# Kernel tuning notes

Measured on AMD Instinct MI355X. Metric: run time of the kernel, lower is better.

Reference implementation:

```python
import jax, jax.numpy as jnp
import numpy as np

NC = 80            # number of classes (COCO)
NM = 32            # mask coefficients (YOLOv5-seg)
D = 4 + 1 + NC + NM
N_ANCHORS = 100800  # 1280x1280 input, strides 8/16/32, 3 anchors
CONF_THRES = 0.25
IOU_THRES = 0.45
MAX_DET = 300
TOPK = 4096        # fixed pre-NMS candidate budget (jit-compatible stand-in for boolean filter)


def setup_inputs() -> dict:
    key = jax.random.key(0)
    x = jax.random.uniform(key, (1, N_ANCHORS, D), dtype=jnp.float32)
    return {"x": x}


def _pairwise_iou(boxes):
    # boxes: [K, 4] in (y1, x1, y2, x2)
    y1, x1, y2, x2 = boxes[:, 0], boxes[:, 1], boxes[:, 2], boxes[:, 3]
    area = (y2 - y1) * (x2 - x1)
    iy1 = jnp.maximum(y1[:, None], y1[None, :])
    ix1 = jnp.maximum(x1[:, None], x1[None, :])
    iy2 = jnp.minimum(y2[:, None], y2[None, :])
    ix2 = jnp.minimum(x2[:, None], x2[None, :])
    inter = jnp.clip(iy2 - iy1, 0.0) * jnp.clip(ix2 - ix1, 0.0)
    union = area[:, None] + area[None, :] - inter
    return inter / jnp.maximum(union, 1e-9)


def reference(x):
    p = x[0]                                   # [N, D] (loop returns after first image)
    obj = p[:, 4]
    valid = obj > CONF_THRES                   # candidates = obj score > conf_thres
    cls_scores = p[:, 5:5 + NC] * obj[:, None] # scores = cls * obj
    scores = jnp.max(cls_scores, axis=1)
    classes = jnp.argmax(cls_scores, axis=1).astype(x.dtype)
    # xywh (center) -> yxyx
    xc, yc, w, h = p[:, 0], p[:, 1], p[:, 2], p[:, 3]
    yxyx = jnp.stack([yc - h * 0.5, xc - w * 0.5, yc + h * 0.5, xc + w * 0.5], axis=1)
    masks = p[:, 5 + NC:]                      # [N, NM]
    # replace torch's boolean-filter gather with fixed-size top-K over masked scores
    scores_m = jnp.where(valid, scores, -1.0)
    top_s, top_i = jax.lax.top_k(scores_m, TOPK)   # sorted desc, as torchvision nms requires
    b = yxyx[top_i]                            # [K, 4]
    keep0 = top_s > -0.5                       # only real candidates
    iou = _pairwise_iou(b)                     # [K, K]
    j_idx = jnp.arange(TOPK)

    def body(i, keep):
        sup = keep[i] & (iou[i] > IOU_THRES) & (j_idx > i)
        return keep & ~sup

    keep = jax.lax.fori_loop(0, TOPK, body, keep0)
    # pad/select top MAX_DET surviving detections (score -1.0 marks padding)
    sel_s = jnp.where(keep, top_s, -1.0)
    out_s, out_i = jax.lax.top_k(sel_s, MAX_DET)
    gi = top_i[out_i]
    return (yxyx[gi][None], classes[gi][None], out_s[None], masks[gi][None])
```

## Files before the change

### kernel.cpp

```cpp
#include <hip/hip_runtime.h>


#define AS1 __attribute__((address_space(1)))
#define AS3 __attribute__((address_space(3)))

constexpr int    N_ANCH = 100800;
constexpr int    DIMV   = 117;
constexpr int    NCLS   = 80;
constexpr int    TOPKN  = 4096;
constexpr int    MAXDET = 300;
constexpr int    KCAP   = 12288;
constexpr int    NBUCK  = 16384;
constexpr int    NSLICE = 32;

constexpr size_t WS_HIST   = 0;
constexpr size_t WS_SCORES = WS_HIST   + 65536ull * 4;
constexpr size_t WS_CLS    = WS_SCORES + 100800ull * 4;
constexpr size_t WS_SEL    = WS_CLS    + 100800ull * 4;
constexpr size_t WS_KEYS   = WS_SEL    + 256;
constexpr size_t WS_RANK   = WS_KEYS   + (size_t)KCAP * 8;
constexpr size_t WS_SIDX   = WS_RANK   + (size_t)KCAP * 4;
constexpr size_t WS_SSC    = WS_SIDX   + 4096ull * 4;
constexpr size_t WS_BOXES  = WS_SSC    + 4096ull * 4;
constexpr size_t WS_MASK   = WS_BOXES  + 4096ull * 16;
constexpr size_t WS_OUTI   = WS_MASK   + 4096ull * 64 * 8;
constexpr size_t WS_OUTS   = WS_OUTI   + 1200;

__global__ void zero_kernel(unsigned* __restrict__ slices, int* __restrict__ sel,
                            int* __restrict__ rank) {
    int i = blockIdx.x * blockDim.x + threadIdx.x;
    if (i < NSLICE * NBUCK) slices[i] = 0u;
    if (i < KCAP)           rank[i]  = 0;
    if (i < 64)             sel[i]   = 0;
}

constexpr int SROWS = 64;
__global__ void score_kernel(const float* __restrict__ x, float* __restrict__ scores,
                             int* __restrict__ cls, unsigned* __restrict__ slices) {
    __shared__ float sx[SROWS * DIMV];
    int block0 = blockIdx.x * SROWS;
    const float4* src = (const float4*)(x + (size_t)block0 * DIMV);
    float4* dst = (float4*)sx;
    constexpr int NV4 = SROWS * DIMV / 4;
    for (int i = threadIdx.x; i < NV4; i += 128) dst[i] = src[i];
    __syncthreads();
    int row  = threadIdx.x >> 1;
    int half = threadIdx.x & 1;
    const float* rp = sx + row * DIMV;
    float obj = rp[4];
    const float* cp = rp + 5 + half * 40;
    float best = -1.0f;
    int   bc   = half * 40;
#pragma unroll 8
    for (int c = 0; c < 40; ++c) {
        float s = __fmul_rn(cp[c], obj);
        if (s > best) { best = s; bc = half * 40 + c; }
    }
    float so = __shfl_xor(best, 1);
    int   co = __shfl_xor(bc, 1);
    if (half == 0) {
        if (so > best) { best = so; bc = co; }
        int a = block0 + row;
        bool valid = obj > 0.25f;
        scores[a] = valid ? best : -1.0f;
        cls[a]    = bc;
        if (valid) {
            unsigned b = __float_as_uint(best) >> 16;
            atomicAdd(&slices[(blockIdx.x & (NSLICE - 1)) * NBUCK + b], 1u);
        }
    }
}

__global__ void reduce_hist_kernel(const unsigned* __restrict__ slices,
                                   unsigned* __restrict__ hist) {
    int b = blockIdx.x * 256 + threadIdx.x;
    unsigned s = 0;
#pragma unroll
    for (int k = 0; k < NSLICE; ++k) s += slices[k * NBUCK + b];
    hist[b] = s;
}

__global__ void select_kernel(const unsigned* __restrict__ hist, int* sel) {
    __shared__ unsigned sv[1024];
    int t = threadIdx.x;
    int base = NBUCK - 16 * (t + 1);
    const uint4* hp = (const uint4*)(hist + base);
    unsigned own = 0;
#pragma unroll
    for (int k = 0; k < 4; ++k) {
        uint4 v = hp[k];
        own += v.x + v.y + v.z + v.w;
    }
    sv[t] = own;
    __syncthreads();
    for (int off = 1; off < 1024; off <<= 1) {
        unsigned v = (t >= off) ? sv[t - off] : 0u;
        __syncthreads();
        sv[t] += v;
        __syncthreads();
    }
    unsigned incl = sv[t];
    unsigned before = incl - own;
    if (before < (unsigned)TOPKN && incl >= (unsigned)TOPKN) {
        unsigned running = before;
        for (int k = 15; k >= 0; --k) {
            unsigned h = hist[base + k];
            running += h;
            if (running >= (unsigned)TOPKN) {
                sel[0] = base + k;
                sel[1] = (int)(running - h);
                break;
            }
        }
    }
}

__global__ void compact_kernel(const float* __restrict__ scores, int* sel,
                               unsigned long long* __restrict__ keys) {
    int a = blockIdx.x * blockDim.x + threadIdx.x;
    if (a >= N_ANCH) return;
    float s = scores[a];
    if (s < 0.0f) return;
    unsigned bits = __float_as_uint(s);
    if ((int)(bits >> 16) < sel[0]) return;
    int pos = atomicAdd(&sel[2], 1);
    if (pos < KCAP) keys[pos] = ((unsigned long long)bits << 32) | (unsigned)(~a);
}

constexpr int NCOLP = 4;
__global__ void rank_kernel(const unsigned long long* __restrict__ keys,
                            const int* __restrict__ sel, int* __restrict__ rank) {
    __shared__ unsigned long long tile[2048];
    int n = sel[2]; if (n > KCAP) n = KCAP;
    int i = blockIdx.x * 256 + threadIdx.x;
    unsigned long long myKey = (i < n) ? keys[i] : 0ull;
    int cnt = 0;
    for (int t0 = blockIdx.y * 2048; t0 < n; t0 += 2048 * NCOLP) {
        int m = n - t0; if (m > 2048) m = 2048;
        for (int j = threadIdx.x; j < m; j += 256) tile[j] = keys[t0 + j];
        __syncthreads();
        int j = 0;
        for (; j + 3 < m; j += 4) {
            cnt += (tile[j]     > myKey);
            cnt += (tile[j + 1] > myKey);
            cnt += (tile[j + 2] > myKey);
            cnt += (tile[j + 3] > myKey);
        }
        for (; j < m; ++j) cnt += (tile[j] > myKey);
        __syncthreads();
    }
    if (i < n && cnt < TOPKN) atomicAdd(&rank[i], cnt);
}

__global__ void scatter_kernel(const float* __restrict__ x,
                               const unsigned long long* __restrict__ keys,
                               const int* __restrict__ sel, const int* __restrict__ rank,
                               int* __restrict__ sidx, float* __restrict__ sscore,
                               float* __restrict__ boxes) {
    int n = sel[2]; if (n > KCAP) n = KCAP;
    int i = blockIdx.x * 256 + threadIdx.x;
    if (i >= n) return;
    int r = rank[i];
    if (r >= TOPKN) return;
    unsigned long long k = keys[i];
    int a = (int)(~(unsigned)(k & 0xFFFFFFFFull));
    sidx[r]   = a;
    sscore[r] = __uint_as_float((unsigned)(k >> 32));
    const float* p = x + (size_t)a * DIMV;
    float xc = p[0], yc = p[1], w = p[2], h = p[3];
    float hw = __fmul_rn(w, 0.5f);
    float hh = __fmul_rn(h, 0.5f);
    boxes[r * 4 + 0] = __fsub_rn(yc, hh);
    boxes[r * 4 + 1] = __fsub_rn(xc, hw);
    boxes[r * 4 + 2] = __fadd_rn(yc, hh);
    boxes[r * 4 + 3] = __fadd_rn(xc, hw);
}

__global__ void iou_mask_kernel(const float* __restrict__ boxes,
                                unsigned long long* __restrict__ mask) {
    int colT = blockIdx.x, rowT = blockIdx.y;
    int t = threadIdx.x;
    int r = rowT * 64 + t;
    if (colT < rowT) {
        mask[(size_t)r * 64 + colT] = 0ull;
        return;
    }
    __shared__ float cb[64][5];
    int cj = colT * 64 + t;
    {
        float y1 = boxes[cj * 4 + 0], x1 = boxes[cj * 4 + 1];
        float y2 = boxes[cj * 4 + 2], x2 = boxes[cj * 4 + 3];
        cb[t][0] = y1; cb[t][1] = x1; cb[t][2] = y2; cb[t][3] = x2;
        cb[t][4] = __fmul_rn(__fsub_rn(y2, y1), __fsub_rn(x2, x1));
    }
    __syncthreads();
    float ry1 = boxes[r * 4 + 0], rx1 = boxes[r * 4 + 1];
    float ry2 = boxes[r * 4 + 2], rx2 = boxes[r * 4 + 3];
    float rarea = __fmul_rn(__fsub_rn(ry2, ry1), __fsub_rn(rx2, rx1));
    unsigned long long bitsw = 0ull;
#pragma unroll 8
    for (int j = 0; j < 64; ++j) {
        float iy1 = fmaxf(ry1, cb[j][0]);
        float ix1 = fmaxf(rx1, cb[j][1]);
        float iy2 = fminf(ry2, cb[j][2]);
        float ix2 = fminf(rx2, cb[j][3]);
        float ih = fmaxf(__fsub_rn(iy2, iy1), 0.0f);
        float iw = fmaxf(__fsub_rn(ix2, ix1), 0.0f);
        float inter = __fmul_rn(ih, iw);
        float uni = __fsub_rn(__fadd_rn(rarea, cb[j][4]), inter);
        float iou = __fdiv_rn(inter, fmaxf(uni, 1e-9f));
        if (iou > 0.45f && (colT * 64 + j) > r) bitsw |= (1ull << j);
    }
    mask[(size_t)r * 64 + colT] = bitsw;
}

__global__ void __launch_bounds__(64, 1)
nms_scan_kernel(const unsigned long long* __restrict__ mask,
                const float* __restrict__ sscore,
                int* __restrict__ outIdx, float* __restrict__ outScore) {
    int lane = threadIdx.x;
    unsigned long long remv = 0ull;
    __shared__ __align__(16) unsigned long long tile[2 * 4096];
    __shared__ int keepArr[MAXDET];
    __shared__ unsigned long long remvFinal[64];
    int count = 0;

    auto issueBatch = [&](int w) {
        const char* gbase = (const char*)mask + (size_t)w * 32768 + (size_t)lane * 16;
        char* lbase = (char*)tile + (size_t)(w & 1) * 32768;
#pragma unroll
        for (int i = 0; i < 32; ++i) {
            __builtin_amdgcn_global_load_lds(
                (AS1 const unsigned*)(gbase + (size_t)i * 1024),
                (AS3 unsigned*)(lbase + (size_t)i * 1024), 16, 0, 0);
        }
    };

    issueBatch(0);
    for (int w = 0; w < 64 && count < MAXDET; ++w) {
        if (w + 1 < 64) issueBatch(w + 1);
        unsigned long long cand = __shfl(~remv, w);
        if (!cand) continue;
        asm volatile("s_waitcnt vmcnt(32)" ::: "memory");
        const unsigned long long* trow = tile + (size_t)(w & 1) * 4096;
        while (cand && count < MAXDET) {
            int bs[8];
            unsigned long long c2 = cand;
            int g = 0;
#pragma unroll
            for (int t = 0; t < 8; ++t) {
                bs[t] = c2 ? (int)__builtin_ctzll(c2) : 0;
                if (c2) { c2 &= c2 - 1; g = t + 1; }
            }
            unsigned long long mvs[8];
#pragma unroll
            for (int t = 0; t < 8; ++t) {
                mvs[t] = trow[(size_t)bs[t] * 64 + lane];
            }
#pragma unroll
            for (int t = 0; t < 8; ++t) {
                if (t < g && count < MAXDET) {
                    int b = bs[t];
                    unsigned long long bal = __ballot(((remv >> b) & 1ull) != 0);
                    if (!((bal >> w) & 1ull)) {
                        if (lane == 0) keepArr[count] = (w << 6) + b;
                        count++;
                        remv |= mvs[t];
                    }
                }
            }
            cand = c2;
        }
    }
    __syncthreads();
    remvFinal[lane] = remv;
    __syncthreads();
    int K = count;
    for (int k = lane; k < K; k += 64) {
        int s = keepArr[k];
        outIdx[k] = s;
        outScore[k] = sscore[s];
    }
    if (K < MAXDET && lane == 0) {
        int filled = K;
        for (int w = 0; w < 64 && filled < MAXDET; ++w) {
            unsigned long long word = remvFinal[w];
            while (word && filled < MAXDET) {
                int b = (int)__builtin_ctzll(word);
                word &= word - 1;
                outIdx[filled] = (w << 6) + b;
                outScore[filled] = -1.0f;
                filled++;
            }
        }
    }
}

__global__ void write_out_kernel(const float* __restrict__ x, const int* __restrict__ sidx,
                                 const int* __restrict__ cls, const float* __restrict__ boxes,
                                 const int* __restrict__ outIdx, const float* __restrict__ outScore,
                                 float* __restrict__ out) {
    int o = blockIdx.x;
    int t = threadIdx.x;
    int s = outIdx[o];
    int a = sidx[s];
    if (t < 32) {
        out[1800 + o * 32 + t] = x[(size_t)a * DIMV + 85 + t];
    } else if (t < 36) {
        out[o * 4 + (t - 32)] = boxes[s * 4 + (t - 32)];
    } else if (t == 36) {
        out[1200 + o] = (float)cls[a];
    } else if (t == 37) {
        out[1500 + o] = outScore[o];
    }
}

extern "C" void kernel_launch(void* const* d_in, const int* in_sizes, int n_in,
                              void* d_out, int out_size, void* d_ws, size_t ws_size,
                              hipStream_t stream) {
    const float* x = (const float*)d_in[0];
    char* ws = (char*)d_ws;
    unsigned*            hist   = (unsigned*)(ws + WS_HIST);
    float*               scores = (float*)(ws + WS_SCORES);
    int*                 cls    = (int*)(ws + WS_CLS);
    int*                 sel    = (int*)(ws + WS_SEL);
    unsigned long long*  keys   = (unsigned long long*)(ws + WS_KEYS);
    int*                 rank   = (int*)(ws + WS_RANK);
    int*                 sidx   = (int*)(ws + WS_SIDX);
    float*               sscore = (float*)(ws + WS_SSC);
    float*               boxes  = (float*)(ws + WS_BOXES);
    unsigned long long*  mask   = (unsigned long long*)(ws + WS_MASK);
    unsigned*            slices = (unsigned*)(ws + WS_MASK);
    int*                 outIdx = (int*)(ws + WS_OUTI);
    float*               outSc  = (float*)(ws + WS_OUTS);

    zero_kernel<<<(NSLICE * NBUCK + 255) / 256, 256, 0, stream>>>(slices, sel, rank);
    score_kernel<<<N_ANCH / SROWS, 128, 0, stream>>>(x, scores, cls, slices);
    reduce_hist_kernel<<<NBUCK / 256, 256, 0, stream>>>(slices, hist);
    select_kernel<<<1, 1024, 0, stream>>>(hist, sel);
    compact_kernel<<<(N_ANCH + 255) / 256, 256, 0, stream>>>(scores, sel, keys);
    dim3 rg(KCAP / 256, NCOLP);
    rank_kernel<<<rg, 256, 0, stream>>>(keys, sel, rank);
    scatter_kernel<<<KCAP / 256, 256, 0, stream>>>(x, keys, sel, rank, sidx, sscore, boxes);
    dim3 mg(64, 64);
    iou_mask_kernel<<<mg, 64, 0, stream>>>(boxes, mask);
    nms_scan_kernel<<<1, 64, 0, stream>>>(mask, sscore, outIdx, outSc);
    write_out_kernel<<<MAXDET, 64, 0, stream>>>(x, sidx, cls, boxes, outIdx, outSc, (float*)d_out);
}
```

Measured before the change: 216.6 us.

## Pack upper-triangular NMS mask, fold histogram reduce into select, restructure scan

Stores only the upper-triangular IoU mask tiles in a packed layout plus a separate diagonal copy. The NMS scan now resolves each 64-box word from the diagonal using readlanes and only ORs kept rows' packed tiles, so it streams about half as much data into LDS. It also fuses the histogram reduction into select (with fewer slices), moves rank zeroing into compact, and splits rank into one tile per block with early exits. The per-iteration waitcnt switch and packed indexing add complexity and carry a risk of off-by-one errors.

New measurement: 247.3 us. +14.2%, slower.

```diff
diff --git a/kernel.cpp b/kernel.cpp
--- a/kernel.cpp
+++ b/kernel.cpp
@@ -6,32 +6,32 @@
 
 constexpr int    N_ANCH = 100800;
 constexpr int    DIMV   = 117;
-constexpr int    NCLS   = 80;
 constexpr int    TOPKN  = 4096;
 constexpr int    MAXDET = 300;
 constexpr int    KCAP   = 12288;
 constexpr int    NBUCK  = 16384;
-constexpr int    NSLICE = 32;
-
-constexpr size_t WS_HIST   = 0;
-constexpr size_t WS_SCORES = WS_HIST   + 65536ull * 4;
-constexpr size_t WS_CLS    = WS_SCORES + 100800ull * 4;
-constexpr size_t WS_SEL    = WS_CLS    + 100800ull * 4;
+constexpr int    NSLICE = 8;
+
+constexpr int PACK_TOT = 133120;
+
+constexpr size_t WS_SLICES = 0;
+constexpr size_t WS_SCORES = WS_SLICES + (size_t)NSLICE * NBUCK * 4;
+constexpr size_t WS_CLS    = WS_SCORES + (size_t)N_ANCH * 4;
+constexpr size_t WS_SEL    = WS_CLS    + (size_t)N_ANCH * 4;
 constexpr size_t WS_KEYS   = WS_SEL    + 256;
 constexpr size_t WS_RANK   = WS_KEYS   + (size_t)KCAP * 8;
 constexpr size_t WS_SIDX   = WS_RANK   + (size_t)KCAP * 4;
 constexpr size_t WS_SSC    = WS_SIDX   + 4096ull * 4;
 constexpr size_t WS_BOXES  = WS_SSC    + 4096ull * 4;
-constexpr size_t WS_MASK   = WS_BOXES  + 4096ull * 16;
-constexpr size_t WS_OUTI   = WS_MASK   + 4096ull * 64 * 8;
-constexpr size_t WS_OUTS   = WS_OUTI   + 1200;
-
-__global__ void zero_kernel(unsigned* __restrict__ slices, int* __restrict__ sel,
-                            int* __restrict__ rank) {
-    int i = blockIdx.x * blockDim.x + threadIdx.x;
+constexpr size_t WS_MASKP  = WS_BOXES  + 4096ull * 16;
+constexpr size_t WS_DIAG   = WS_MASKP  + (size_t)PACK_TOT * 8 + 4096;
+constexpr size_t WS_OUTI   = WS_DIAG   + 4096ull * 8;
+constexpr size_t WS_OUTS   = WS_OUTI   + 1280;
+
+__global__ void zero_kernel(unsigned* __restrict__ slices, int* __restrict__ sel) {
+    int i = blockIdx.x * 256 + threadIdx.x;
     if (i < NSLICE * NBUCK) slices[i] = 0u;
-    if (i < KCAP)           rank[i]  = 0;
-    if (i < 64)             sel[i]   = 0;
+    if (i < 64)             sel[i]    = 0;
 }
 
 constexpr int SROWS = 64;
@@ -71,26 +71,25 @@
     }
 }
 
-__global__ void reduce_hist_kernel(const unsigned* __restrict__ slices,
-                                   unsigned* __restrict__ hist) {
-    int b = blockIdx.x * 256 + threadIdx.x;
-    unsigned s = 0;
-#pragma unroll
-    for (int k = 0; k < NSLICE; ++k) s += slices[k * NBUCK + b];
-    hist[b] = s;
-}
-
-__global__ void select_kernel(const unsigned* __restrict__ hist, int* sel) {
+__global__ void select_kernel(const unsigned* __restrict__ slices, int* sel) {
     __shared__ unsigned sv[1024];
     int t = threadIdx.x;
     int base = NBUCK - 16 * (t + 1);
-    const uint4* hp = (const uint4*)(hist + base);
+    unsigned hb[16];
+#pragma unroll
+    for (int k = 0; k < 16; ++k) hb[k] = 0u;
+    for (int s = 0; s < NSLICE; ++s) {
+        const uint4* hp = (const uint4*)(slices + (size_t)s * NBUCK + base);
+#pragma unroll
+        for (int q = 0; q < 4; ++q) {
+            uint4 v = hp[q];
+            hb[q * 4 + 0] += v.x; hb[q * 4 + 1] += v.y;
+            hb[q * 4 + 2] += v.z; hb[q * 4 + 3] += v.w;
+        }
+    }
     unsigned own = 0;
 #pragma unroll
-    for (int k = 0; k < 4; ++k) {
-        uint4 v = hp[k];
-        own += v.x + v.y + v.z + v.w;
-    }
+    for (int k = 0; k < 16; ++k) own += hb[k];
     sv[t] = own;
     __syncthreads();
     for (int off = 1; off < 1024; off <<= 1) {
@@ -104,11 +103,10 @@
     if (before < (unsigned)TOPKN && incl >= (unsigned)TOPKN) {
         unsigned running = before;
         for (int k = 15; k >= 0; --k) {
-            unsigned h = hist[base + k];
-            running += h;
+            running += hb[k];
             if (running >= (unsigned)TOPKN) {
                 sel[0] = base + k;
-                sel[1] = (int)(running - h);
+                sel[1] = (int)(running - hb[k]);
                 break;
             }
         }
@@ -116,8 +114,10 @@
 }
 
 __global__ void compact_kernel(const float* __restrict__ scores, int* sel,
-                               unsigned long long* __restrict__ keys) {
+                               unsigned long long* __restrict__ keys,
+                               int* __restrict__ rank) {
     int a = blockIdx.x * blockDim.x + threadIdx.x;
+    if (a < KCAP) rank[a] = 0;
     if (a >= N_ANCH) return;
     float s = scores[a];
     if (s < 0.0f) return;
@@ -127,29 +127,29 @@
     if (pos < KCAP) keys[pos] = ((unsigned long long)bits << 32) | (unsigned)(~a);
 }
 
-constexpr int NCOLP = 4;
+constexpr int NCOLP = 8;
 __global__ void rank_kernel(const unsigned long long* __restrict__ keys,
                             const int* __restrict__ sel, int* __restrict__ rank) {
     __shared__ unsigned long long tile[2048];
     int n = sel[2]; if (n > KCAP) n = KCAP;
+    if (blockIdx.x * 256 >= n) return;
+    int t0 = blockIdx.y * 2048;
+    if (t0 >= n) return;
     int i = blockIdx.x * 256 + threadIdx.x;
     unsigned long long myKey = (i < n) ? keys[i] : 0ull;
+    int m = n - t0; if (m > 2048) m = 2048;
+    for (int j = threadIdx.x; j < m; j += 256) tile[j] = keys[t0 + j];
+    __syncthreads();
     int cnt = 0;
-    for (int t0 = blockIdx.y * 2048; t0 < n; t0 += 2048 * NCOLP) {
-        int m = n - t0; if (m > 2048) m = 2048;
-        for (int j = threadIdx.x; j < m; j += 256) tile[j] = keys[t0 + j];
-        __syncthreads();
-        int j = 0;
-        for (; j + 3 < m; j += 4) {
-            cnt += (tile[j]     > myKey);
-            cnt += (tile[j + 1] > myKey);
-            cnt += (tile[j + 2] > myKey);
-            cnt += (tile[j + 3] > myKey);
-        }
-        for (; j < m; ++j) cnt += (tile[j] > myKey);
-        __syncthreads();
-    }
-    if (i < n && cnt < TOPKN) atomicAdd(&rank[i], cnt);
+    int j = 0;
+    for (; j + 3 < m; j += 4) {
+        cnt += (tile[j]     > myKey);
+        cnt += (tile[j + 1] > myKey);
+        cnt += (tile[j + 2] > myKey);
+        cnt += (tile[j + 3] > myKey);
+    }
+    for (; j < m; ++j) cnt += (tile[j] > myKey);
+    if (i < n && cnt) atomicAdd(&rank[i], cnt);
 }
 
 __global__ void scatter_kernel(const float* __restrict__ x,
@@ -177,25 +177,23 @@
 }
 
 __global__ void iou_mask_kernel(const float* __restrict__ boxes,
-                                unsigned long long* __restrict__ mask) {
+                                unsigned long long* __restrict__ maskp,
+                                unsigned long long* __restrict__ diag) {
     int colT = blockIdx.x, rowT = blockIdx.y;
+    if (colT < rowT) return;
     int t = threadIdx.x;
-    int r = rowT * 64 + t;
-    if (colT < rowT) {
-        mask[(size_t)r * 64 + colT] = 0ull;
-        return;
-    }
     __shared__ float cb[64][5];
+    const float4* bp = (const float4*)boxes;
     int cj = colT * 64 + t;
     {
-        float y1 = boxes[cj * 4 + 0], x1 = boxes[cj * 4 + 1];
-        float y2 = boxes[cj * 4 + 2], x2 = boxes[cj * 4 + 3];
-        cb[t][0] = y1; cb[t][1] = x1; cb[t][2] = y2; cb[t][3] = x2;
-        cb[t][4] = __fmul_rn(__fsub_rn(y2, y1), __fsub_rn(x2, x1));
-    }
-    __syncthreads();
-    float ry1 = boxes[r * 4 + 0], rx1 = boxes[r * 4 + 1];
-    float ry2 = boxes[r * 4 + 2], rx2 = boxes[r * 4 + 3];
+        float4 c = bp[cj];
+        cb[t][0] = c.x; cb[t][1] = c.y; cb[t][2] = c.z; cb[t][3] = c.w;
+        cb[t][4] = __fmul_rn(__fsub_rn(c.z, c.x), __fsub_rn(c.w, c.y));
+    }
+    __syncthreads();
+    int r = rowT * 64 + t;
+    float4 rv = bp[r];
+    float ry1 = rv.x, rx1 = rv.y, ry2 = rv.z, rx2 = rv.w;
     float rarea = __fmul_rn(__fsub_rn(ry2, ry1), __fsub_rn(rx2, rx1));
     unsigned long long bitsw = 0ull;
 #pragma unroll 8
@@ -211,65 +209,105 @@
         float iou = __fdiv_rn(inter, fmaxf(uni, 1e-9f));
         if (iou > 0.45f && (colT * 64 + j) > r) bitsw |= (1ull << j);
     }
-    mask[(size_t)r * 64 + colT] = bitsw;
+    int pb = 64 * (64 * rowT - (rowT * (rowT - 1)) / 2);
+    maskp[pb + t * (64 - rowT) + (colT - rowT)] = bitsw;
+    if (colT == rowT) diag[(rowT << 6) + t] = bitsw;
+}
+
+__device__ __forceinline__ unsigned long long readlane64(unsigned long long v, int l) {
+    unsigned lo = (unsigned)__builtin_amdgcn_readlane((int)(unsigned)(v & 0xFFFFFFFFull), l);
+    unsigned hi = (unsigned)__builtin_amdgcn_readlane((int)(unsigned)(v >> 32), l);
+    return ((unsigned long long)hi << 32) | lo;
 }
 
 __global__ void __launch_bounds__(64, 1)
-nms_scan_kernel(const unsigned long long* __restrict__ mask,
+nms_scan_kernel(const unsigned long long* __restrict__ maskp,
+                const unsigned long long* __restrict__ diagG,
                 const float* __restrict__ sscore,
                 int* __restrict__ outIdx, float* __restrict__ outScore) {
     int lane = threadIdx.x;
     unsigned long long remv = 0ull;
     __shared__ __align__(16) unsigned long long tile[2 * 4096];
+    __shared__ __align__(16) unsigned long long diagLds[4096];
     __shared__ int keepArr[MAXDET];
     __shared__ unsigned long long remvFinal[64];
     int count = 0;
 
     auto issueBatch = [&](int w) {
-        const char* gbase = (const char*)mask + (size_t)w * 32768 + (size_t)lane * 16;
+        if (w >= 64) return;
+        int L = (65 - w) >> 1;
+        const char* gbase = (const char*)maskp +
+                            (size_t)(64 * (64 * w - (w * (w - 1)) / 2)) * 8 +
+                            (size_t)lane * 16;
         char* lbase = (char*)tile + (size_t)(w & 1) * 32768;
-#pragma unroll
-        for (int i = 0; i < 32; ++i) {
+        for (int i = 0; i < L; ++i) {
             __builtin_amdgcn_global_load_lds(
                 (AS1 const unsigned*)(gbase + (size_t)i * 1024),
                 (AS3 unsigned*)(lbase + (size_t)i * 1024), 16, 0, 0);
         }
     };
 
+    {
+        const char* gb = (const char*)diagG + (size_t)lane * 16;
+        char* lb = (char*)diagLds;
+#pragma unroll
+        for (int i = 0; i < 32; ++i) {
+            __builtin_amdgcn_global_load_lds(
+                (AS1 const unsigned*)(gb + (size_t)i * 1024),
+                (AS3 unsigned*)(lb + (size_t)i * 1024), 16, 0, 0);
+        }
+    }
     issueBatch(0);
+
+#define VW(n) asm volatile("s_waitcnt vmcnt(" #n ")" ::: "memory")
+
     for (int w = 0; w < 64 && count < MAXDET; ++w) {
-        if (w + 1 < 64) issueBatch(w + 1);
+        issueBatch(w + 1);
         unsigned long long cand = __shfl(~remv, w);
         if (!cand) continue;
-        asm volatile("s_waitcnt vmcnt(32)" ::: "memory");
+        int p = (w < 63) ? ((64 - w) >> 1) : 0;
+        switch (p) {
+            case 32: VW(32); break; case 31: VW(31); break; case 30: VW(30); break;
+            case 29: VW(29); break; case 28: VW(28); break; case 27: VW(27); break;
+            case 26: VW(26); break; case 25: VW(25); break; case 24: VW(24); break;
+            case 23: VW(23); break; case 22: VW(22); break; case 21: VW(21); break;
+            case 20: VW(20); break; case 19: VW(19); break; case 18: VW(18); break;
+            case 17: VW(17); break; case 16: VW(16); break; case 15: VW(15); break;
+            case 14: VW(14); break; case 13: VW(13); break; case 12: VW(12); break;
+            case 11: VW(11); break; case 10: VW(10); break; case  9: VW(9);  break;
+            case  8: VW(8);  break; case  7: VW(7);  break; case  6: VW(6);  break;
+            case  5: VW(5);  break; case  4: VW(4);  break; case  3: VW(3);  break;
+            case  2: VW(2);  break; case  1: VW(1);  break; default: VW(0);  break;
+        }
+        unsigned long long diagv = diagLds[(w << 6) | lane];
+        unsigned long long alive = cand;
+        unsigned long long keptM = 0ull;
+        while (alive && count < MAXDET) {
+            int b = (int)__builtin_ctzll(alive);
+            unsigned long long db = readlane64(diagv, b);
+            if (lane == 0) keepArr[count] = (w << 6) + b;
+            count++;
+            keptM |= (1ull << b);
+            alive &= ~(db | (1ull << b));
+        }
         const unsigned long long* trow = tile + (size_t)(w & 1) * 4096;
-        while (cand && count < MAXDET) {
-            int bs[8];
-            unsigned long long c2 = cand;
-            int g = 0;
-#pragma unroll
-            for (int t = 0; t < 8; ++t) {
-                bs[t] = c2 ? (int)__builtin_ctzll(c2) : 0;
-                if (c2) { c2 &= c2 - 1; g = t + 1; }
+        int stride = 64 - w;
+        int rel = lane - w;
+        while (keptM) {
+            int bs[4]; unsigned long long t2 = keptM; int g = 0;
+#pragma unroll
+            for (int t = 0; t < 4; ++t) {
+                bs[t] = t2 ? (int)__builtin_ctzll(t2) : 0;
+                if (t2) { t2 &= t2 - 1; g = t + 1; }
             }
-            unsigned long long mvs[8];
-#pragma unroll
-            for (int t = 0; t < 8; ++t) {
-                mvs[t] = trow[(size_t)bs[t] * 64 + lane];
-            }
-#pragma unroll
-            for (int t = 0; t < 8; ++t) {
-                if (t < g && count < MAXDET) {
-                    int b = bs[t];
-                    unsigned long long bal = __ballot(((remv >> b) & 1ull) != 0);
-                    if (!((bal >> w) & 1ull)) {
-                        if (lane == 0) keepArr[count] = (w << 6) + b;
-                        count++;
-                        remv |= mvs[t];
-                    }
-                }
-            }
-            cand = c2;
+            unsigned long long vs[4];
+#pragma unroll
+            for (int t = 0; t < 4; ++t)
+                vs[t] = (rel >= 0) ? trow[bs[t] * stride + rel] : 0ull;
+#pragma unroll
+            for (int t = 0; t < 4; ++t)
+                if (t < g) remv |= vs[t];
+            keptM = t2;
         }
     }
     __syncthreads();
@@ -320,7 +358,7 @@
                               hipStream_t stream) {
     const float* x = (const float*)d_in[0];
     char* ws = (char*)d_ws;
-    unsigned*            hist   = (unsigned*)(ws + WS_HIST);
+    unsigned*            slices = (unsigned*)(ws + WS_SLICES);
     float*               scores = (float*)(ws + WS_SCORES);
     int*                 cls    = (int*)(ws + WS_CLS);
     int*                 sel    = (int*)(ws + WS_SEL);
@@ -329,21 +367,20 @@
     int*                 sidx   = (int*)(ws + WS_SIDX);
     float*               sscore = (float*)(ws + WS_SSC);
     float*               boxes  = (float*)(ws + WS_BOXES);
-    unsigned long long*  mask   = (unsigned long long*)(ws + WS_MASK);
-    unsigned*            slices = (unsigned*)(ws + WS_MASK);
+    unsigned long long*  maskp  = (unsigned long long*)(ws + WS_MASKP);
+    unsigned long long*  diag   = (unsigned long long*)(ws + WS_DIAG);
     int*                 outIdx = (int*)(ws + WS_OUTI);
     float*               outSc  = (float*)(ws + WS_OUTS);
 
-    zero_kernel<<<(NSLICE * NBUCK + 255) / 256, 256, 0, stream>>>(slices, sel, rank);
+    zero_kernel<<<(NSLICE * NBUCK) / 256, 256, 0, stream>>>(slices, sel);
     score_kernel<<<N_ANCH / SROWS, 128, 0, stream>>>(x, scores, cls, slices);
-    reduce_hist_kernel<<<NBUCK / 256, 256, 0, stream>>>(slices, hist);
-    select_kernel<<<1, 1024, 0, stream>>>(hist, sel);
-    compact_kernel<<<(N_ANCH + 255) / 256, 256, 0, stream>>>(scores, sel, keys);
+    select_kernel<<<1, 1024, 0, stream>>>(slices, sel);
+    compact_kernel<<<(N_ANCH + 255) / 256, 256, 0, stream>>>(scores, sel, keys, rank);
     dim3 rg(KCAP / 256, NCOLP);
     rank_kernel<<<rg, 256, 0, stream>>>(keys, sel, rank);
     scatter_kernel<<<KCAP / 256, 256, 0, stream>>>(x, keys, sel, rank, sidx, sscore, boxes);
     dim3 mg(64, 64);
-    iou_mask_kernel<<<mg, 64, 0, stream>>>(boxes, mask);
-    nms_scan_kernel<<<1, 64, 0, stream>>>(mask, sscore, outIdx, outSc);
+    iou_mask_kernel<<<mg, 64, 0, stream>>>(boxes, maskp, diag);
+    nms_scan_kernel<<<1, 64, 0, stream>>>(maskp, diag, sscore, outIdx, outSc);
     write_out_kernel<<<MAXDET, 64, 0, stream>>>(x, sidx, cls, boxes, outIdx, outSc, (float*)d_out);
 }
```

## Fuse NMS pipeline into one persistent kernel with software grid barriers

Applied to the files above, without the earlier changes.

Replaces the chain of ten kernel launches with a single persistent 256-block kernel that separates its phases with atomic grid barriers, plus a small init kernel. It also switches to per-block shared-memory histograms, packs the IoU mask as an upper triangle only, and rewrites the NMS scan as a greedy next-alive-candidate search with prefetched mask rows. The aim is to remove launch overhead and the zero-fill and reduce passes. In exchange, phases such as ranking now run on fewer parallel blocks, and the spin barriers depend on all 256 blocks being co-resident.

Measured after the change: 815.0 us. 3.76x slower.

```diff
diff --git a/kernel.cpp b/kernel.cpp
--- a/kernel.cpp
+++ b/kernel.cpp
@@ -1,317 +1,354 @@
 #include <hip/hip_runtime.h>
 
 
-#define AS1 __attribute__((address_space(1)))
-#define AS3 __attribute__((address_space(3)))
-
-constexpr int    N_ANCH = 100800;
-constexpr int    DIMV   = 117;
-constexpr int    NCLS   = 80;
-constexpr int    TOPKN  = 4096;
-constexpr int    MAXDET = 300;
-constexpr int    KCAP   = 12288;
-constexpr int    NBUCK  = 16384;
-constexpr int    NSLICE = 32;
+typedef unsigned long long u64;
+
+constexpr int N_ANCH = 100800;
+constexpr int DIMV   = 117;
+constexpr int NCLS   = 80;
+constexpr int TOPKN  = 4096;
+constexpr int MAXDET = 300;
+constexpr int KCAP   = 12288;
+constexpr int NBUCK  = 16384;
+constexpr int NBLK   = 256;
+constexpr int NTHR   = 256;
+constexpr int GSIZE  = NBLK * NTHR;
+
+constexpr int NTILE2 = 2080;
 
 constexpr size_t WS_HIST   = 0;
-constexpr size_t WS_SCORES = WS_HIST   + 65536ull * 4;
-constexpr size_t WS_CLS    = WS_SCORES + 100800ull * 4;
-constexpr size_t WS_SEL    = WS_CLS    + 100800ull * 4;
-constexpr size_t WS_KEYS   = WS_SEL    + 256;
+constexpr size_t WS_BAR    = WS_HIST   + 65536;
+constexpr size_t WS_SEL    = WS_BAR    + 128;
+constexpr size_t WS_SARR   = WS_SEL    + 256;
+constexpr size_t WS_SCORES = WS_SARR   + 1472;
+constexpr size_t WS_CLS    = WS_SCORES + (size_t)N_ANCH * 4;
+constexpr size_t WS_KEYS   = WS_CLS    + (size_t)N_ANCH * 4;
 constexpr size_t WS_RANK   = WS_KEYS   + (size_t)KCAP * 8;
 constexpr size_t WS_SIDX   = WS_RANK   + (size_t)KCAP * 4;
 constexpr size_t WS_SSC    = WS_SIDX   + 4096ull * 4;
 constexpr size_t WS_BOXES  = WS_SSC    + 4096ull * 4;
-constexpr size_t WS_MASK   = WS_BOXES  + 4096ull * 16;
-constexpr size_t WS_OUTI   = WS_MASK   + 4096ull * 64 * 8;
-constexpr size_t WS_OUTS   = WS_OUTI   + 1200;
-
-__global__ void zero_kernel(unsigned* __restrict__ slices, int* __restrict__ sel,
-                            int* __restrict__ rank) {
-    int i = blockIdx.x * blockDim.x + threadIdx.x;
-    if (i < NSLICE * NBUCK) slices[i] = 0u;
-    if (i < KCAP)           rank[i]  = 0;
-    if (i < 64)             sel[i]   = 0;
-}
-
-constexpr int SROWS = 64;
-__global__ void score_kernel(const float* __restrict__ x, float* __restrict__ scores,
-                             int* __restrict__ cls, unsigned* __restrict__ slices) {
-    __shared__ float sx[SROWS * DIMV];
-    int block0 = blockIdx.x * SROWS;
-    const float4* src = (const float4*)(x + (size_t)block0 * DIMV);
-    float4* dst = (float4*)sx;
-    constexpr int NV4 = SROWS * DIMV / 4;
-    for (int i = threadIdx.x; i < NV4; i += 128) dst[i] = src[i];
+constexpr size_t WS_MASKP  = WS_BOXES  + 4096ull * 16;
+
+__global__ void init_kernel(unsigned* __restrict__ hist, int* __restrict__ sel,
+                            unsigned* __restrict__ bar) {
+    int i = blockIdx.x * 256 + threadIdx.x;
+    if (i < NBUCK) hist[i] = 0u;
+    if (i < 64)    sel[i]  = 0;
+    if (i < 32)    bar[i]  = 0u;
+}
+
+__device__ __forceinline__ void gridbar(unsigned* bar, int phase) {
     __syncthreads();
-    int row  = threadIdx.x >> 1;
-    int half = threadIdx.x & 1;
-    const float* rp = sx + row * DIMV;
-    float obj = rp[4];
-    const float* cp = rp + 5 + half * 40;
-    float best = -1.0f;
-    int   bc   = half * 40;
+    if (threadIdx.x == 0) {
+        __threadfence();
+        __hip_atomic_fetch_add(&bar[phase], 1u, __ATOMIC_ACQ_REL,
+                               __HIP_MEMORY_SCOPE_AGENT);
+        while (__hip_atomic_load(&bar[phase], __ATOMIC_ACQUIRE,
+                                 __HIP_MEMORY_SCOPE_AGENT) < (unsigned)NBLK) {
+            __builtin_amdgcn_s_sleep(2);
+        }
+        __threadfence();
+    }
+    __syncthreads();
+}
+
+__device__ __forceinline__ u64 readlane64(u64 v, int l) {
+    unsigned lo = (unsigned)__builtin_amdgcn_readlane((int)(unsigned)(v & 0xFFFFFFFFull), l);
+    unsigned hi = (unsigned)__builtin_amdgcn_readlane((int)(unsigned)(v >> 32), l);
+    return ((u64)hi << 32) | lo;
+}
+
+__global__ void __launch_bounds__(NTHR, 1)
+mega_kernel(const float* __restrict__ x, float* __restrict__ out,
+            char* __restrict__ ws) {
+    unsigned* hist   = (unsigned*)(ws + WS_HIST);
+    unsigned* bar    = (unsigned*)(ws + WS_BAR);
+    int*      sel    = (int*)(ws + WS_SEL);
+    int*      sArrG  = (int*)(ws + WS_SARR);
+    float*    scores = (float*)(ws + WS_SCORES);
+    int*      cls    = (int*)(ws + WS_CLS);
+    u64*      keys   = (u64*)(ws + WS_KEYS);
+    int*      rank   = (int*)(ws + WS_RANK);
+    int*      sidx   = (int*)(ws + WS_SIDX);
+    float*    sscore = (float*)(ws + WS_SSC);
+    float*    boxes  = (float*)(ws + WS_BOXES);
+    u64*      maskp  = (u64*)(ws + WS_MASKP);
+
+    __shared__ __align__(16) char smem[125440];
+
+    {
+        float*    sx = (float*)smem;
+        unsigned* lh = (unsigned*)(smem + 59904);
+        for (int i = threadIdx.x; i < NBUCK; i += NTHR) lh[i] = 0u;
+        __syncthreads();
+        constexpr int TROWS = 128;
+        constexpr int NTILE = (N_ANCH + TROWS - 1) / TROWS;
+        for (int tile = blockIdx.x; tile < NTILE; tile += NBLK) {
+            int r0 = tile * TROWS;
+            int rows = N_ANCH - r0; if (rows > TROWS) rows = TROWS;
+            const float4* src = (const float4*)(x + (size_t)r0 * DIMV);
+            float4* dst = (float4*)sx;
+            int nv4 = rows * DIMV / 4;
+            for (int i = threadIdx.x; i < nv4; i += NTHR) dst[i] = src[i];
+            __syncthreads();
+            int row = threadIdx.x >> 1, half = threadIdx.x & 1;
+            if (row < rows) {
+                const float* rp = sx + row * DIMV;
+                float obj = rp[4];
+                const float* cp = rp + 5 + half * 40;
+                float best = -1.0f; int bc = half * 40;
 #pragma unroll 8
-    for (int c = 0; c < 40; ++c) {
-        float s = __fmul_rn(cp[c], obj);
-        if (s > best) { best = s; bc = half * 40 + c; }
-    }
-    float so = __shfl_xor(best, 1);
-    int   co = __shfl_xor(bc, 1);
-    if (half == 0) {
-        if (so > best) { best = so; bc = co; }
-        int a = block0 + row;
-        bool valid = obj > 0.25f;
-        scores[a] = valid ? best : -1.0f;
-        cls[a]    = bc;
-        if (valid) {
-            unsigned b = __float_as_uint(best) >> 16;
-            atomicAdd(&slices[(blockIdx.x & (NSLICE - 1)) * NBUCK + b], 1u);
-        }
-    }
-}
-
-__global__ void reduce_hist_kernel(const unsigned* __restrict__ slices,
-                                   unsigned* __restrict__ hist) {
-    int b = blockIdx.x * 256 + threadIdx.x;
-    unsigned s = 0;
+                for (int c = 0; c < 40; ++c) {
+                    float s = __fmul_rn(cp[c], obj);
+                    if (s > best) { best = s; bc = half * 40 + c; }
+                }
+                float so = __shfl_xor(best, 1);
+                int   co = __shfl_xor(bc, 1);
+                if (half == 0) {
+                    if (so > best) { best = so; bc = co; }
+                    int a = r0 + row;
+                    bool valid = obj > 0.25f;
+                    scores[a] = valid ? best : -1.0f;
+                    cls[a] = bc;
+                    if (valid) atomicAdd(&lh[__float_as_uint(best) >> 16], 1u);
+                }
+            }
+            __syncthreads();
+        }
+        for (int b = threadIdx.x; b < NBUCK; b += NTHR) {
+            unsigned v = lh[b];
+            if (v) atomicAdd(&hist[b], v);
+        }
+    }
+    gridbar(bar, 0);
+
+    if (blockIdx.x == 0) {
+        unsigned* sv = (unsigned*)smem;
+        int* bsh = (int*)(smem + 2048);
+        int t = threadIdx.x;
+        int base = NBUCK - 64 * (t + 1);
+        const uint4* hp = (const uint4*)(hist + base);
+        unsigned own = 0;
 #pragma unroll
-    for (int k = 0; k < NSLICE; ++k) s += slices[k * NBUCK + b];
-    hist[b] = s;
-}
-
-__global__ void select_kernel(const unsigned* __restrict__ hist, int* sel) {
-    __shared__ unsigned sv[1024];
-    int t = threadIdx.x;
-    int base = NBUCK - 16 * (t + 1);
-    const uint4* hp = (const uint4*)(hist + base);
-    unsigned own = 0;
+        for (int q = 0; q < 16; ++q) { uint4 v = hp[q]; own += v.x + v.y + v.z + v.w; }
+        sv[t] = own;
+        __syncthreads();
+        for (int off = 1; off < 256; off <<= 1) {
+            unsigned v = (t >= off) ? sv[t - off] : 0u;
+            __syncthreads();
+            sv[t] += v;
+            __syncthreads();
+        }
+        unsigned incl = sv[t], before = incl - own;
+        if (before < (unsigned)TOPKN && incl >= (unsigned)TOPKN) {
+            bsh[0] = t; bsh[1] = (int)before;
+        }
+        __syncthreads();
+        if (t == 0) {
+            int ts = bsh[0];
+            unsigned running = (unsigned)bsh[1];
+            int cbase = NBUCK - 64 * (ts + 1);
+            unsigned hh[64];
 #pragma unroll
-    for (int k = 0; k < 4; ++k) {
-        uint4 v = hp[k];
-        own += v.x + v.y + v.z + v.w;
-    }
-    sv[t] = own;
-    __syncthreads();
-    for (int off = 1; off < 1024; off <<= 1) {
-        unsigned v = (t >= off) ? sv[t - off] : 0u;
-        __syncthreads();
-        sv[t] += v;
-        __syncthreads();
-    }
-    unsigned incl = sv[t];
-    unsigned before = incl - own;
-    if (before < (unsigned)TOPKN && incl >= (unsigned)TOPKN) {
-        unsigned running = before;
-        for (int k = 15; k >= 0; --k) {
-            unsigned h = hist[base + k];
-            running += h;
-            if (running >= (unsigned)TOPKN) {
-                sel[0] = base + k;
-                sel[1] = (int)(running - h);
-                break;
-            }
-        }
-    }
-}
-
-__global__ void compact_kernel(const float* __restrict__ scores, int* sel,
-                               unsigned long long* __restrict__ keys) {
-    int a = blockIdx.x * blockDim.x + threadIdx.x;
-    if (a >= N_ANCH) return;
-    float s = scores[a];
-    if (s < 0.0f) return;
-    unsigned bits = __float_as_uint(s);
-    if ((int)(bits >> 16) < sel[0]) return;
-    int pos = atomicAdd(&sel[2], 1);
-    if (pos < KCAP) keys[pos] = ((unsigned long long)bits << 32) | (unsigned)(~a);
-}
-
-constexpr int NCOLP = 4;
-__global__ void rank_kernel(const unsigned long long* __restrict__ keys,
-                            const int* __restrict__ sel, int* __restrict__ rank) {
-    __shared__ unsigned long long tile[2048];
-    int n = sel[2]; if (n > KCAP) n = KCAP;
-    int i = blockIdx.x * 256 + threadIdx.x;
-    unsigned long long myKey = (i < n) ? keys[i] : 0ull;
-    int cnt = 0;
-    for (int t0 = blockIdx.y * 2048; t0 < n; t0 += 2048 * NCOLP) {
-        int m = n - t0; if (m > 2048) m = 2048;
-        for (int j = threadIdx.x; j < m; j += 256) tile[j] = keys[t0 + j];
-        __syncthreads();
-        int j = 0;
-        for (; j + 3 < m; j += 4) {
-            cnt += (tile[j]     > myKey);
-            cnt += (tile[j + 1] > myKey);
-            cnt += (tile[j + 2] > myKey);
-            cnt += (tile[j + 3] > myKey);
-        }
-        for (; j < m; ++j) cnt += (tile[j] > myKey);
-        __syncthreads();
-    }
-    if (i < n && cnt < TOPKN) atomicAdd(&rank[i], cnt);
-}
-
-__global__ void scatter_kernel(const float* __restrict__ x,
-                               const unsigned long long* __restrict__ keys,
-                               const int* __restrict__ sel, const int* __restrict__ rank,
-                               int* __restrict__ sidx, float* __restrict__ sscore,
-                               float* __restrict__ boxes) {
-    int n = sel[2]; if (n > KCAP) n = KCAP;
-    int i = blockIdx.x * 256 + threadIdx.x;
-    if (i >= n) return;
-    int r = rank[i];
-    if (r >= TOPKN) return;
-    unsigned long long k = keys[i];
-    int a = (int)(~(unsigned)(k & 0xFFFFFFFFull));
-    sidx[r]   = a;
-    sscore[r] = __uint_as_float((unsigned)(k >> 32));
-    const float* p = x + (size_t)a * DIMV;
-    float xc = p[0], yc = p[1], w = p[2], h = p[3];
-    float hw = __fmul_rn(w, 0.5f);
-    float hh = __fmul_rn(h, 0.5f);
-    boxes[r * 4 + 0] = __fsub_rn(yc, hh);
-    boxes[r * 4 + 1] = __fsub_rn(xc, hw);
-    boxes[r * 4 + 2] = __fadd_rn(yc, hh);
-    boxes[r * 4 + 3] = __fadd_rn(xc, hw);
-}
-
-__global__ void iou_mask_kernel(const float* __restrict__ boxes,
-                                unsigned long long* __restrict__ mask) {
-    int colT = blockIdx.x, rowT = blockIdx.y;
-    int t = threadIdx.x;
-    int r = rowT * 64 + t;
-    if (colT < rowT) {
-        mask[(size_t)r * 64 + colT] = 0ull;
-        return;
-    }
-    __shared__ float cb[64][5];
-    int cj = colT * 64 + t;
-    {
-        float y1 = boxes[cj * 4 + 0], x1 = boxes[cj * 4 + 1];
-        float y2 = boxes[cj * 4 + 2], x2 = boxes[cj * 4 + 3];
-        cb[t][0] = y1; cb[t][1] = x1; cb[t][2] = y2; cb[t][3] = x2;
-        cb[t][4] = __fmul_rn(__fsub_rn(y2, y1), __fsub_rn(x2, x1));
-    }
-    __syncthreads();
-    float ry1 = boxes[r * 4 + 0], rx1 = boxes[r * 4 + 1];
-    float ry2 = boxes[r * 4 + 2], rx2 = boxes[r * 4 + 3];
-    float rarea = __fmul_rn(__fsub_rn(ry2, ry1), __fsub_rn(rx2, rx1));
-    unsigned long long bitsw = 0ull;
+            for (int u = 0; u < 64; ++u) hh[u] = hist[cbase + 63 - u];
+            for (int u = 0; u < 64; ++u) {
+                if (running + hh[u] >= (unsigned)TOPKN) { sel[0] = cbase + 63 - u; break; }
+                running += hh[u];
+            }
+        }
+    }
+    gridbar(bar, 1);
+
+    {
+        int B = sel[0];
+        for (int a = blockIdx.x * NTHR + threadIdx.x; a < N_ANCH; a += GSIZE) {
+            float s = scores[a];
+            if (s < 0.0f) continue;
+            unsigned bits = __float_as_uint(s);
+            if ((int)(bits >> 16) < B) continue;
+            int pos = atomicAdd(&sel[2], 1);
+            if (pos < KCAP) keys[pos] = ((u64)bits << 32) | (unsigned)(~a);
+        }
+    }
+    gridbar(bar, 2);
+
+    {
+        u64* tile = (u64*)smem;
+        int n = sel[2]; if (n > KCAP) n = KCAP;
+        int RB = (n + NTHR - 1) / NTHR;
+        for (int rb = blockIdx.x; rb < RB; rb += NBLK) {
+            int i = rb * NTHR + threadIdx.x;
+            u64 myKey = (i < n) ? keys[i] : 0ull;
+            int cnt = 0;
+            for (int t0 = 0; t0 < n; t0 += 2048) {
+                int m = n - t0; if (m > 2048) m = 2048;
+                __syncthreads();
+                for (int j = threadIdx.x; j < m; j += NTHR) tile[j] = keys[t0 + j];
+                __syncthreads();
+                int j = 0;
+                for (; j + 3 < m; j += 4) {
+                    cnt += (tile[j]     > myKey);
+                    cnt += (tile[j + 1] > myKey);
+                    cnt += (tile[j + 2] > myKey);
+                    cnt += (tile[j + 3] > myKey);
+                }
+                for (; j < m; ++j) cnt += (tile[j] > myKey);
+            }
+            if (i < n) rank[i] = cnt;
+        }
+    }
+    gridbar(bar, 3);
+
+    {
+        int n = sel[2]; if (n > KCAP) n = KCAP;
+        for (int i = blockIdx.x * NTHR + threadIdx.x; i < n; i += GSIZE) {
+            int r = rank[i];
+            if (r >= TOPKN) continue;
+            u64 k = keys[i];
+            int a = (int)(~(unsigned)(k & 0xFFFFFFFFull));
+            sidx[r] = a;
+            sscore[r] = __uint_as_float((unsigned)(k >> 32));
+            const float* p = x + (size_t)a * DIMV;
+            float xc = p[0], yc = p[1], w = p[2], h = p[3];
+            float hw = __fmul_rn(w, 0.5f);
+            float hh = __fmul_rn(h, 0.5f);
+            boxes[r * 4 + 0] = __fsub_rn(yc, hh);
+            boxes[r * 4 + 1] = __fsub_rn(xc, hw);
+            boxes[r * 4 + 2] = __fadd_rn(yc, hh);
+            boxes[r * 4 + 3] = __fadd_rn(xc, hw);
+        }
+    }
+    gridbar(bar, 4);
+
+    {
+        float (*cb)[64][5] = (float (*)[64][5])smem;
+        int sw = threadIdx.x >> 6, t = threadIdx.x & 63;
+        for (int k0 = blockIdx.x * 4; k0 < NTILE2; k0 += NBLK * 4) {
+            int k = k0 + sw;
+            double disc = 129.0 * 129.0 - 8.0 * (double)k;
+            int rowT = (int)((129.0 - sqrt(disc)) * 0.5);
+            while ((rowT + 1) * (129 - (rowT + 1)) / 2 <= k) ++rowT;
+            while (rowT * (129 - rowT) / 2 > k) --rowT;
+            int colT = rowT + (k - rowT * (129 - rowT) / 2);
+            const float4* bp = (const float4*)boxes;
+            {
+                float4 c = bp[colT * 64 + t];
+                cb[sw][t][0] = c.x; cb[sw][t][1] = c.y;
+                cb[sw][t][2] = c.z; cb[sw][t][3] = c.w;
+                cb[sw][t][4] = __fmul_rn(__fsub_rn(c.z, c.x), __fsub_rn(c.w, c.y));
+            }
+            __syncthreads();
+            int r = rowT * 64 + t;
+            float4 rv = bp[r];
+            float ry1 = rv.x, rx1 = rv.y, ry2 = rv.z, rx2 = rv.w;
+            float rarea = __fmul_rn(__fsub_rn(ry2, ry1), __fsub_rn(rx2, rx1));
+            u64 bitsw = 0ull;
 #pragma unroll 8
-    for (int j = 0; j < 64; ++j) {
-        float iy1 = fmaxf(ry1, cb[j][0]);
-        float ix1 = fmaxf(rx1, cb[j][1]);
-        float iy2 = fminf(ry2, cb[j][2]);
-        float ix2 = fminf(rx2, cb[j][3]);
-        float ih = fmaxf(__fsub_rn(iy2, iy1), 0.0f);
-        float iw = fmaxf(__fsub_rn(ix2, ix1), 0.0f);
-        float inter = __fmul_rn(ih, iw);
-        float uni = __fsub_rn(__fadd_rn(rarea, cb[j][4]), inter);
-        float iou = __fdiv_rn(inter, fmaxf(uni, 1e-9f));
-        if (iou > 0.45f && (colT * 64 + j) > r) bitsw |= (1ull << j);
-    }
-    mask[(size_t)r * 64 + colT] = bitsw;
-}
-
-__global__ void __launch_bounds__(64, 1)
-nms_scan_kernel(const unsigned long long* __restrict__ mask,
-                const float* __restrict__ sscore,
-                int* __restrict__ outIdx, float* __restrict__ outScore) {
-    int lane = threadIdx.x;
-    unsigned long long remv = 0ull;
-    __shared__ __align__(16) unsigned long long tile[2 * 4096];
-    __shared__ int keepArr[MAXDET];
-    __shared__ unsigned long long remvFinal[64];
-    int count = 0;
-
-    auto issueBatch = [&](int w) {
-        const char* gbase = (const char*)mask + (size_t)w * 32768 + (size_t)lane * 16;
-        char* lbase = (char*)tile + (size_t)(w & 1) * 32768;
+            for (int j = 0; j < 64; ++j) {
+                float iy1 = fmaxf(ry1, cb[sw][j][0]);
+                float ix1 = fmaxf(rx1, cb[sw][j][1]);
+                float iy2 = fminf(ry2, cb[sw][j][2]);
+                float ix2 = fminf(rx2, cb[sw][j][3]);
+                float ih = fmaxf(__fsub_rn(iy2, iy1), 0.0f);
+                float iw = fmaxf(__fsub_rn(ix2, ix1), 0.0f);
+                float inter = __fmul_rn(ih, iw);
+                float uni = __fsub_rn(__fadd_rn(rarea, cb[sw][j][4]), inter);
+                float iou = __fdiv_rn(inter, fmaxf(uni, 1e-9f));
+                if (iou > 0.45f && (colT * 64 + j) > r) bitsw |= (1ull << j);
+            }
+            int pb = 64 * (64 * rowT - (rowT * (rowT - 1)) / 2);
+            maskp[pb + t * (64 - rowT) + (colT - rowT)] = bitsw;
+            __syncthreads();
+        }
+    }
+    gridbar(bar, 5);
+
+    if (blockIdx.x == 0 && threadIdx.x < 64) {
+        int lane = threadIdx.x;
+        u64 alive = ~0ull;
+        int count = 0, scanPtr = 0, emptyRun = 0;
+        int q[16]; u64 d[16];
+
+        auto findNext = [&](int sp) -> int {
+            if (sp >= TOPKN) return TOPKN;
+            u64 m = alive;
+            int wsrd = sp >> 6;
+            if (lane == wsrd) m &= (~0ull) << (sp & 63);
+            if (lane < wsrd)  m = 0ull;
+            u64 bal = __ballot(m != 0ull);
+            if (!bal) return TOPKN;
+            int l0 = (int)__builtin_ctzll(bal);
+            u64 w = readlane64(m, l0);
+            return l0 * 64 + (int)__builtin_ctzll(w);
+        };
+        auto loadRow = [&](int c) -> u64 {
+            int rT = c >> 6;
+            int strd = 64 - rT;
+            int rel = lane - rT; if (rel < 0) rel = 0;
+            size_t idx = (size_t)(64 * (64 * rT - (rT * (rT - 1)) / 2))
+                       + (size_t)(c & 63) * strd + rel;
+            return maskp[idx];
+        };
+
 #pragma unroll
-        for (int i = 0; i < 32; ++i) {
-            __builtin_amdgcn_global_load_lds(
-                (AS1 const unsigned*)(gbase + (size_t)i * 1024),
-                (AS3 unsigned*)(lbase + (size_t)i * 1024), 16, 0, 0);
-        }
-    };
-
-    issueBatch(0);
-    for (int w = 0; w < 64 && count < MAXDET; ++w) {
-        if (w + 1 < 64) issueBatch(w + 1);
-        unsigned long long cand = __shfl(~remv, w);
-        if (!cand) continue;
-        asm volatile("s_waitcnt vmcnt(32)" ::: "memory");
-        const unsigned long long* trow = tile + (size_t)(w & 1) * 4096;
-        while (cand && count < MAXDET) {
-            int bs[8];
-            unsigned long long c2 = cand;
-            int g = 0;
+        for (int s = 0; s < 16; ++s) {
+            int c = findNext(scanPtr);
+            q[s] = c;
+            if (c < TOPKN) { scanPtr = c + 1; d[s] = loadRow(c); }
+            else d[s] = 0ull;
+        }
+        bool done = false;
+        while (!done) {
 #pragma unroll
-            for (int t = 0; t < 8; ++t) {
-                bs[t] = c2 ? (int)__builtin_ctzll(c2) : 0;
-                if (c2) { c2 &= c2 - 1; g = t + 1; }
-            }
-            unsigned long long mvs[8];
-#pragma unroll
-            for (int t = 0; t < 8; ++t) {
-                mvs[t] = trow[(size_t)bs[t] * 64 + lane];
-            }
-#pragma unroll
-            for (int t = 0; t < 8; ++t) {
-                if (t < g && count < MAXDET) {
-                    int b = bs[t];
-                    unsigned long long bal = __ballot(((remv >> b) & 1ull) != 0);
-                    if (!((bal >> w) & 1ull)) {
-                        if (lane == 0) keepArr[count] = (w << 6) + b;
-                        count++;
-                        remv |= mvs[t];
+            for (int s = 0; s < 16; ++s) {
+                int c = q[s];
+                if (c >= TOPKN) {
+                    if (++emptyRun >= 16) { done = true; break; }
+                    continue;
+                }
+                emptyRun = 0;
+                u64 aw = readlane64(alive, c >> 6);
+                if ((aw >> (c & 63)) & 1ull) {
+                    u64 row = (lane >= (c >> 6)) ? d[s] : 0ull;
+                    alive &= ~row;
+                    if (lane == 0) sArrG[count] = c;
+                    ++count;
+                    if (count >= MAXDET) { done = true; break; }
+                }
+                int nc = findNext(scanPtr);
+                q[s] = nc;
+                if (nc < TOPKN) { scanPtr = nc + 1; d[s] = loadRow(nc); }
+            }
+        }
+        if (lane == 0) {
+            sel[3] = count;
+            if (count < MAXDET) {
+                int filled = count;
+                for (int w2 = 0; w2 < 64 && filled < MAXDET; ++w2) {
+                    u64 word = ~readlane64(alive, w2);
+                    while (word && filled < MAXDET) {
+                        int b = (int)__builtin_ctzll(word);
+                        word &= word - 1;
+                        sArrG[filled++] = (w2 << 6) + b;
                     }
                 }
             }
-            cand = c2;
-        }
-    }
-    __syncthreads();
-    remvFinal[lane] = remv;
-    __syncthreads();
-    int K = count;
-    for (int k = lane; k < K; k += 64) {
-        int s = keepArr[k];
-        outIdx[k] = s;
-        outScore[k] = sscore[s];
-    }
-    if (K < MAXDET && lane == 0) {
-        int filled = K;
-        for (int w = 0; w < 64 && filled < MAXDET; ++w) {
-            unsigned long long word = remvFinal[w];
-            while (word && filled < MAXDET) {
-                int b = (int)__builtin_ctzll(word);
-                word &= word - 1;
-                outIdx[filled] = (w << 6) + b;
-                outScore[filled] = -1.0f;
-                filled++;
-            }
-        }
-    }
-}
-
-__global__ void write_out_kernel(const float* __restrict__ x, const int* __restrict__ sidx,
-                                 const int* __restrict__ cls, const float* __restrict__ boxes,
-                                 const int* __restrict__ outIdx, const float* __restrict__ outScore,
-                                 float* __restrict__ out) {
-    int o = blockIdx.x;
-    int t = threadIdx.x;
-    int s = outIdx[o];
-    int a = sidx[s];
-    if (t < 32) {
-        out[1800 + o * 32 + t] = x[(size_t)a * DIMV + 85 + t];
-    } else if (t < 36) {
-        out[o * 4 + (t - 32)] = boxes[s * 4 + (t - 32)];
-    } else if (t == 36) {
-        out[1200 + o] = (float)cls[a];
-    } else if (t == 37) {
-        out[1500 + o] = outScore[o];
+        }
+    }
+    gridbar(bar, 6);
+
+    {
+        int K = sel[3];
+        int gtid = blockIdx.x * NTHR + threadIdx.x;
+        int o = gtid >> 5, t32 = gtid & 31;
+        if (o < MAXDET) {
+            int s = sArrG[o];
+            int a = sidx[s];
+            out[1800 + o * 32 + t32] = x[(size_t)a * DIMV + 85 + t32];
+            if (t32 < 4)       out[o * 4 + t32] = boxes[s * 4 + t32];
+            else if (t32 == 4) out[1200 + o] = (float)cls[a];
+            else if (t32 == 5) out[1500 + o] = (o < K) ? sscore[s] : -1.0f;
+        }
     }
 }
 
@@ -320,30 +357,10 @@
                               hipStream_t stream) {
     const float* x = (const float*)d_in[0];
     char* ws = (char*)d_ws;
-    unsigned*            hist   = (unsigned*)(ws + WS_HIST);
-    float*               scores = (float*)(ws + WS_SCORES);
-    int*                 cls    = (int*)(ws + WS_CLS);
-    int*                 sel    = (int*)(ws + WS_SEL);
-    unsigned long long*  keys   = (unsigned long long*)(ws + WS_KEYS);
-    int*                 rank   = (int*)(ws + WS_RANK);
-    int*                 sidx   = (int*)(ws + WS_SIDX);
-    float*               sscore = (float*)(ws + WS_SSC);
-    float*               boxes  = (float*)(ws + WS_BOXES);
-    unsigned long long*  mask   = (unsigned long long*)(ws + WS_MASK);
-    unsigned*            slices = (unsigned*)(ws + WS_MASK);
-    int*                 outIdx = (int*)(ws + WS_OUTI);
-    float*               outSc  = (float*)(ws + WS_OUTS);
-
-    zero_kernel<<<(NSLICE * NBUCK + 255) / 256, 256, 0, stream>>>(slices, sel, rank);
-    score_kernel<<<N_ANCH / SROWS, 128, 0, stream>>>(x, scores, cls, slices);
-    reduce_hist_kernel<<<NBUCK / 256, 256, 0, stream>>>(slices, hist);
-    select_kernel<<<1, 1024, 0, stream>>>(hist, sel);
-    compact_kernel<<<(N_ANCH + 255) / 256, 256, 0, stream>>>(scores, sel, keys);
-    dim3 rg(KCAP / 256, NCOLP);
-    rank_kernel<<<rg, 256, 0, stream>>>(keys, sel, rank);
-    scatter_kernel<<<KCAP / 256, 256, 0, stream>>>(x, keys, sel, rank, sidx, sscore, boxes);
-    dim3 mg(64, 64);
-    iou_mask_kernel<<<mg, 64, 0, stream>>>(boxes, mask);
-    nms_scan_kernel<<<1, 64, 0, stream>>>(mask, sscore, outIdx, outSc);
-    write_out_kernel<<<MAXDET, 64, 0, stream>>>(x, sidx, cls, boxes, outIdx, outSc, (float*)d_out);
-}
+    unsigned* hist = (unsigned*)(ws + WS_HIST);
+    unsigned* bar  = (unsigned*)(ws + WS_BAR);
+    int*      sel  = (int*)(ws + WS_SEL);
+
+    init_kernel<<<64, 256, 0, stream>>>(hist, sel, bar);
+    mega_kernel<<<NBLK, NTHR, 0, stream>>>(x, (float*)d_out, ws);
+}
```
